# Optimization experiments

Hardware: AMD Instinct MI355X
Metric: run time of the kernel (lower is better)

Reference implementation:

```python
import jax, jax.numpy as jnp
import numpy as np

RADIUS = 0.2  # radius_cutoff
EPS_H = 1e-6
EPS_T = 1e-8
NUM_KNOTS = 16


def setup_inputs() -> dict:
    key = jax.random.key(0)
    ks = jax.random.split(key, 10)
    B, N, C = 2, 48 * 48, 16
    x = jax.random.normal(ks[0], (B, N, C), jnp.float32)
    phi_w1 = jax.random.normal(ks[1], (4, 32), jnp.float32) * 0.5
    phi_b1 = jax.random.normal(ks[2], (32,), jnp.float32) * 0.1
    phi_w2 = jax.random.normal(ks[3], (32, 1), jnp.float32) * 0.2
    phi_b2 = jax.random.normal(ks[4], (1,), jnp.float32) * 0.1
    h_w1 = jax.random.normal(ks[5], (2, 32), jnp.float32) * 0.5
    h_b1 = jax.random.normal(ks[6], (32,), jnp.float32) * 0.1
    h_w2 = jax.random.normal(ks[7], (32, 1), jnp.float32) * 0.2
    h_b2 = jax.random.normal(ks[8], (1,), jnp.float32) * 0.1
    S_m = jax.random.normal(ks[9], (NUM_KNOTS,), jnp.float32)
    return dict(x=x, phi_w1=phi_w1, phi_b1=phi_b1, phi_w2=phi_w2, phi_b2=phi_b2,
                h_w1=h_w1, h_b1=h_b1, h_w2=h_w2, h_b2=h_b2, S_m=S_m)


def _radial_spline(r, S_m):
    K = S_m.shape[0]
    knots = jnp.linspace(0.0, 1.0, K)
    r = jnp.clip(r, 0.0, 1.0)
    idx = jnp.clip(jnp.floor(r * (K - 1)).astype(jnp.int32), 0, K - 2)
    t_k = knots[idx]
    t_k1 = knots[idx + 1]
    wr = (r - t_k) / (t_k1 - t_k + EPS_T)
    return (1.0 - wr) * S_m[idx] + wr * S_m[idx + 1]


def reference(x, phi_w1, phi_b1, phi_w2, phi_b2, h_w1, h_b1, h_w2, h_b2, S_m):
    B, N, C = x.shape
    H = int(N ** 0.5)
    lin = jnp.linspace(0.0, 1.0, H)
    gx, gy = jnp.meshgrid(lin, lin, indexing='ij')
    coords = jnp.stack([gx, gy], axis=-1).reshape(N, 2)  # identical for every batch element

    # dense pairwise distances + radius mask  [N, N]
    diff = coords[:, None, :] - coords[None, :, :]
    dist = jnp.sqrt(jnp.sum(diff * diff, axis=-1))
    mask = (dist <= RADIUS).astype(x.dtype)

    # h_net: per-query bandwidth, Softplus(Linear(ReLU(Linear(coords))))  [N]
    h = jax.nn.softplus(jax.nn.relu(coords @ h_w1 + h_b1) @ h_w2 + h_b2)[:, 0]
    r_scaled = dist / (h[:, None] + EPS_H)
    psi = _radial_spline(r_scaled, S_m) * mask  # [N, N]

    # phi_net on all (x_i, y_j) coord pairs; original only fills masked entries,
    # elsewhere phi stays 0 -> dense eval then mask is the same math.  [N, N]
    xy = jnp.concatenate([jnp.broadcast_to(coords[:, None, :], (N, N, 2)),
                          jnp.broadcast_to(coords[None, :, :], (N, N, 2))], axis=-1)
    phi = (jax.nn.relu(xy @ phi_w1 + phi_b1) @ phi_w2 + phi_b2)[..., 0] * mask

    weights = phi * psi  # [N, N], same for every batch element
    norm = jnp.maximum(jnp.sum(mask, axis=-1, keepdims=True), 1.0)  # [N, 1]
    # sum_j weights[i,j] * x[b,j,c] / norm[i]  -- avoids materializing [B,N,N,C]
    out = jnp.einsum('ij,bjc->bic', weights, x) / norm[None, :, :]
    return out
```

## Files before the change

kernel.cpp:

```cpp
#include <hip/hip_runtime.h>
#include <cmath>

namespace {
constexpr int HG = 48;
constexpr int NP = HG * HG;
constexpr int CH = 16;
constexpr int WIN = 19;
constexpr int WIN2 = WIN * WIN;
constexpr float RADIUS = 0.2f;
constexpr float EPS_H = 1e-6f;
constexpr float EPS_T = 1e-8f;
constexpr int KNOTS = 16;
}

__device__ __forceinline__ float lin48(int t) {
    return (t == HG - 1) ? 1.0f : (float)t * (1.0f / (float)(HG - 1));
}

__device__ __forceinline__ float softplus_f(float v) {
    return fmaxf(v, 0.0f) + log1pf(expf(-fabsf(v)));
}

__global__ __launch_bounds__(256)
void si_blocks_kernel(const float* __restrict__ x,
                      const float* __restrict__ phi_w1,
                      const float* __restrict__ phi_b1,
                      const float* __restrict__ phi_w2,
                      const float* __restrict__ phi_b2,
                      const float* __restrict__ h_w1,
                      const float* __restrict__ h_b1,
                      const float* __restrict__ h_w2,
                      const float* __restrict__ h_b2,
                      const float* __restrict__ S_m,
                      float* __restrict__ out)
{
    const int i = blockIdx.x;
    const int tid = threadIdx.x;
    const int ri = i / HG;
    const int ci = i - ri * HG;
    const float xi = lin48(ri);
    const float yi = lin48(ci);

    __shared__ float4 s_q[32];
    __shared__ float  s_Sm[KNOTS];
    __shared__ float  s_h;
    __shared__ float  s_b2;

    if (tid < 32) {
        const float w0 = phi_w1[tid];
        const float w1 = phi_w1[32 + tid];
        const float pre = xi * w0 + yi * w1 + phi_b1[tid];
        s_q[tid] = make_float4(pre, phi_w1[64 + tid], phi_w1[96 + tid], phi_w2[tid]);
    } else if (tid < 48) {
        s_Sm[tid - 32] = S_m[tid - 32];
    } else if (tid == 64) {
        float hv = h_b2[0];
        #pragma unroll
        for (int k = 0; k < 32; ++k) {
            float t = xi * h_w1[k] + yi * h_w1[32 + k] + h_b1[k];
            t = fmaxf(t, 0.0f);
            hv = fmaf(t, h_w2[k], hv);
        }
        s_h = softplus_f(hv) + EPS_H;
        s_b2 = phi_b2[0];
    }
    __syncthreads();

    const float hval = s_h;
    const float b2 = s_b2;

    float acc[2][CH];
    #pragma unroll
    for (int b = 0; b < 2; ++b)
        #pragma unroll
        for (int c = 0; c < CH; ++c) acc[b][c] = 0.0f;
    float cnt = 0.0f;

    for (int t = tid; t < WIN2; t += 256) {
        const int a = t / WIN;
        const int bb = t - a * WIN;
        const int rj = ri + a - 9;
        const int cj = ci + bb - 9;
        if ((unsigned)rj >= (unsigned)HG || (unsigned)cj >= (unsigned)HG) continue;
        const float xj = lin48(rj);
        const float yj = lin48(cj);
        const float dx = xi - xj;
        const float dy = yi - yj;
        const float dist = sqrtf(dx * dx + dy * dy);
        if (dist > RADIUS) continue;
        cnt += 1.0f;

        float p = b2;
        #pragma unroll
        for (int k = 0; k < 32; ++k) {
            const float4 q = s_q[k];
            float hk = fmaf(xj, q.y, fmaf(yj, q.z, q.x));
            hk = fmaxf(hk, 0.0f);
            p = fmaf(hk, q.w, p);
        }

        float r = dist / hval;
        r = fminf(fmaxf(r, 0.0f), 1.0f);
        int idx = (int)(r * (float)(KNOTS - 1));
        idx = idx > (KNOTS - 2) ? (KNOTS - 2) : idx;
        const float tk  = (float)idx * (1.0f / (float)(KNOTS - 1));
        const float tk1 = (idx == KNOTS - 2) ? 1.0f
                        : (float)(idx + 1) * (1.0f / (float)(KNOTS - 1));
        const float wr = (r - tk) / (tk1 - tk + EPS_T);
        const float psi = (1.0f - wr) * s_Sm[idx] + wr * s_Sm[idx + 1];

        const float w = p * psi;
        const int j = rj * HG + cj;
        const float* xp0 = x + (size_t)j * CH;
        const float* xp1 = xp0 + (size_t)NP * CH;
        #pragma unroll
        for (int c = 0; c < CH; ++c) acc[0][c] = fmaf(w, xp0[c], acc[0][c]);
        #pragma unroll
        for (int c = 0; c < CH; ++c) acc[1][c] = fmaf(w, xp1[c], acc[1][c]);
    }

    #pragma unroll
    for (int off = 32; off > 0; off >>= 1) {
        #pragma unroll
        for (int b = 0; b < 2; ++b)
            #pragma unroll
            for (int c = 0; c < CH; ++c)
                acc[b][c] += __shfl_down(acc[b][c], off, 64);
        cnt += __shfl_down(cnt, off, 64);
    }

    __shared__ float s_red[4][33];
    const int lane = tid & 63;
    const int wv = tid >> 6;
    if (lane == 0) {
        #pragma unroll
        for (int b = 0; b < 2; ++b)
            #pragma unroll
            for (int c = 0; c < CH; ++c)
                s_red[wv][b * CH + c] = acc[b][c];
        s_red[wv][32] = cnt;
    }
    __syncthreads();

    if (tid < 32) {
        const float tot = s_red[0][tid] + s_red[1][tid] + s_red[2][tid] + s_red[3][tid];
        const float cn  = s_red[0][32] + s_red[1][32] + s_red[2][32] + s_red[3][32];
        const float norm = fmaxf(cn, 1.0f);
        const int b = tid >> 4;
        const int c = tid & 15;
        out[(size_t)b * NP * CH + (size_t)i * CH + c] = tot / norm;
    }
}

extern "C" void kernel_launch(void* const* d_in, const int* in_sizes, int n_in,
                              void* d_out, int out_size, void* d_ws, size_t ws_size,
                              hipStream_t stream) {
    const float* x      = (const float*)d_in[0];
    const float* phi_w1 = (const float*)d_in[1];
    const float* phi_b1 = (const float*)d_in[2];
    const float* phi_w2 = (const float*)d_in[3];
    const float* phi_b2 = (const float*)d_in[4];
    const float* h_w1   = (const float*)d_in[5];
    const float* h_b1   = (const float*)d_in[6];
    const float* h_w2   = (const float*)d_in[7];
    const float* h_b2   = (const float*)d_in[8];
    const float* S_m    = (const float*)d_in[9];
    float* out          = (float*)d_out;

    si_blocks_kernel<<<dim3(NP), dim3(256), 0, stream>>>(
        x, phi_w1, phi_b1, phi_w2, phi_b2,
        h_w1, h_b1, h_w2, h_b2, S_m, out);
}
```

Before: 100.1 us.

## Map one wavefront per query point and split weight compute from gather

Each 256-thread block now handles four query points, one wavefront each. Every lane computes weights for up to six window candidates without branching, storing the weight and byte offset in shared memory. A second phase has lanes gather float4 slices of x across batch and channel, and reduces the partial sums with a short shuffle tree. This targets idle threads in the 361-entry window, the divergent continue branches, the scalar per-channel loads and the heavy 32-channel shuffle reduction. The cost is more shared memory and registers per thread, plus work spent on masked-out candidates.

```diff
diff --git a/kernel.cpp b/kernel.cpp
--- a/kernel.cpp
+++ b/kernel.cpp
@@ -11,6 +11,8 @@
 constexpr float EPS_H = 1e-6f;
 constexpr float EPS_T = 1e-8f;
 constexpr int KNOTS = 16;
+constexpr int PPB = 4;
+constexpr int NCAND = 6;
 }
 
 __device__ __forceinline__ float lin48(int t) {
@@ -34,121 +36,139 @@
                       const float* __restrict__ S_m,
                       float* __restrict__ out)
 {
-    const int i = blockIdx.x;
-    const int tid = threadIdx.x;
-    const int ri = i / HG;
-    const int ci = i - ri * HG;
+    const int tid  = threadIdx.x;
+    const int lane = tid & 63;
+    const int p    = tid >> 6;
+    const int i    = blockIdx.x * PPB + p;
+    const int ri   = i / HG;
+    const int ci   = i - ri * HG;
     const float xi = lin48(ri);
     const float yi = lin48(ci);
 
-    __shared__ float4 s_q[32];
+    __shared__ float4 s_pq[PPB][32];
+    __shared__ float2 s_wj[PPB][WIN2];
     __shared__ float  s_Sm[KNOTS];
-    __shared__ float  s_h;
-    __shared__ float  s_b2;
 
-    if (tid < 32) {
-        const float w0 = phi_w1[tid];
-        const float w1 = phi_w1[32 + tid];
-        const float pre = xi * w0 + yi * w1 + phi_b1[tid];
-        s_q[tid] = make_float4(pre, phi_w1[64 + tid], phi_w1[96 + tid], phi_w2[tid]);
-    } else if (tid < 48) {
-        s_Sm[tid - 32] = S_m[tid - 32];
-    } else if (tid == 64) {
-        float hv = h_b2[0];
+    if (tid < 128) {
+        const int pb = tid >> 5;
+        const int k  = tid & 31;
+        const int ib = blockIdx.x * PPB + pb;
+        const int rb = ib / HG;
+        const int cb = ib - rb * HG;
+        const float xb = lin48(rb);
+        const float yb = lin48(cb);
+        const float pre = xb * phi_w1[k] + yb * phi_w1[32 + k] + phi_b1[k];
+        s_pq[pb][k] = make_float4(pre, phi_w1[64 + k], phi_w1[96 + k], phi_w2[k]);
+    } else if (tid < 128 + KNOTS) {
+        s_Sm[tid - 128] = S_m[tid - 128];
+    }
+
+    float hval;
+    {
+        const int k = lane & 31;
+        float tk = fmaxf(xi * h_w1[k] + yi * h_w1[32 + k] + h_b1[k], 0.0f) * h_w2[k];
         #pragma unroll
-        for (int k = 0; k < 32; ++k) {
-            float t = xi * h_w1[k] + yi * h_w1[32 + k] + h_b1[k];
-            t = fmaxf(t, 0.0f);
-            hv = fmaf(t, h_w2[k], hv);
-        }
-        s_h = softplus_f(hv) + EPS_H;
-        s_b2 = phi_b2[0];
+        for (int m = 1; m < 32; m <<= 1) tk += __shfl_xor(tk, m, 64);
+        hval = softplus_f(tk + h_b2[0]) + EPS_H;
     }
+    const float b2 = phi_b2[0];
+
     __syncthreads();
 
-    const float hval = s_h;
-    const float b2 = s_b2;
-
-    float acc[2][CH];
-    #pragma unroll
-    for (int b = 0; b < 2; ++b)
-        #pragma unroll
-        for (int c = 0; c < CH; ++c) acc[b][c] = 0.0f;
+    float xj[NCAND], yj[NCAND], pw[NCAND], accp[NCAND];
+    int joff[NCAND];
     float cnt = 0.0f;
 
-    for (int t = tid; t < WIN2; t += 256) {
-        const int a = t / WIN;
-        const int bb = t - a * WIN;
+    #pragma unroll
+    for (int s = 0; s < NCAND; ++s) {
+        const int t  = lane + 64 * s;
+        const bool in = (t < WIN2);
+        const int tt = in ? t : 0;
+        const int a  = tt / WIN;
+        const int bb = tt - a * WIN;
         const int rj = ri + a - 9;
         const int cj = ci + bb - 9;
-        if ((unsigned)rj >= (unsigned)HG || (unsigned)cj >= (unsigned)HG) continue;
-        const float xj = lin48(rj);
-        const float yj = lin48(cj);
-        const float dx = xi - xj;
-        const float dy = yi - yj;
+        const bool valid = in && ((unsigned)rj < (unsigned)HG) && ((unsigned)cj < (unsigned)HG);
+        const int rjc = min(max(rj, 0), HG - 1);
+        const int cjc = min(max(cj, 0), HG - 1);
+        const float xjv = lin48(rjc);
+        const float yjv = lin48(cjc);
+        const float dx = xi - xjv;
+        const float dy = yi - yjv;
         const float dist = sqrtf(dx * dx + dy * dy);
-        if (dist > RADIUS) continue;
-        cnt += 1.0f;
+        const float m = (valid && dist <= RADIUS) ? 1.0f : 0.0f;
+        cnt += m;
 
-        float p = b2;
-        #pragma unroll
-        for (int k = 0; k < 32; ++k) {
-            const float4 q = s_q[k];
-            float hk = fmaf(xj, q.y, fmaf(yj, q.z, q.x));
-            hk = fmaxf(hk, 0.0f);
-            p = fmaf(hk, q.w, p);
-        }
-
-        float r = dist / hval;
-        r = fminf(fmaxf(r, 0.0f), 1.0f);
+        float r = fminf(dist / hval, 1.0f);
         int idx = (int)(r * (float)(KNOTS - 1));
         idx = idx > (KNOTS - 2) ? (KNOTS - 2) : idx;
         const float tk  = (float)idx * (1.0f / (float)(KNOTS - 1));
         const float tk1 = (idx == KNOTS - 2) ? 1.0f
                         : (float)(idx + 1) * (1.0f / (float)(KNOTS - 1));
-        const float wr = (r - tk) / (tk1 - tk + EPS_T);
+        const float wr  = (r - tk) / (tk1 - tk + EPS_T);
         const float psi = (1.0f - wr) * s_Sm[idx] + wr * s_Sm[idx + 1];
 
-        const float w = p * psi;
-        const int j = rj * HG + cj;
-        const float* xp0 = x + (size_t)j * CH;
-        const float* xp1 = xp0 + (size_t)NP * CH;
-        #pragma unroll
-        for (int c = 0; c < CH; ++c) acc[0][c] = fmaf(w, xp0[c], acc[0][c]);
-        #pragma unroll
-        for (int c = 0; c < CH; ++c) acc[1][c] = fmaf(w, xp1[c], acc[1][c]);
+        pw[s]   = psi * m;
+        xj[s]   = xjv;
+        yj[s]   = yjv;
+        accp[s] = b2;
+        joff[s] = (rjc * HG + cjc) * 64;
     }
 
     #pragma unroll
-    for (int off = 32; off > 0; off >>= 1) {
+    for (int m = 1; m < 64; m <<= 1) cnt += __shfl_xor(cnt, m, 64);
+    const float rnorm = 1.0f / fmaxf(cnt, 1.0f);
+
+    #pragma unroll
+    for (int k = 0; k < 32; ++k) {
+        const float4 q = s_pq[p][k];
         #pragma unroll
-        for (int b = 0; b < 2; ++b)
-            #pragma unroll
-            for (int c = 0; c < CH; ++c)
-                acc[b][c] += __shfl_down(acc[b][c], off, 64);
-        cnt += __shfl_down(cnt, off, 64);
+        for (int s = 0; s < NCAND; ++s) {
+            float hk = fmaf(xj[s], q.y, fmaf(yj[s], q.z, q.x));
+            hk = fmaxf(hk, 0.0f);
+            accp[s] = fmaf(hk, q.w, accp[s]);
+        }
     }
 
-    __shared__ float s_red[4][33];
-    const int lane = tid & 63;
-    const int wv = tid >> 6;
-    if (lane == 0) {
-        #pragma unroll
-        for (int b = 0; b < 2; ++b)
-            #pragma unroll
-            for (int c = 0; c < CH; ++c)
-                s_red[wv][b * CH + c] = acc[b][c];
-        s_red[wv][32] = cnt;
+    #pragma unroll
+    for (int s = 0; s < NCAND; ++s) {
+        const int t = lane + 64 * s;
+        if (t < WIN2) {
+            const float w = accp[s] * pw[s] * rnorm;
+            s_wj[p][t] = make_float2(w, __int_as_float(joff[s]));
+        }
     }
+
     __syncthreads();
 
-    if (tid < 32) {
-        const float tot = s_red[0][tid] + s_red[1][tid] + s_red[2][tid] + s_red[3][tid];
-        const float cn  = s_red[0][32] + s_red[1][32] + s_red[2][32] + s_red[3][32];
-        const float norm = fmaxf(cn, 1.0f);
-        const int b = tid >> 4;
-        const int c = tid & 15;
-        out[(size_t)b * NP * CH + (size_t)i * CH + c] = tot / norm;
+    const int rep = (lane >> 3) & 7;
+    const int pc  = lane & 7;
+    const int b   = pc >> 2;
+    const int c4  = pc & 3;
+    const char* xbase = (const char*)x + (size_t)(b * NP * CH + c4 * 4) * 4;
+
+    float4 acc = make_float4(0.0f, 0.0f, 0.0f, 0.0f);
+    #pragma unroll 4
+    for (int t = rep; t < WIN2; t += 8) {
+        const float2 wj = s_wj[p][t];
+        const float4 xv = *(const float4*)(xbase + __float_as_int(wj.y));
+        acc.x = fmaf(wj.x, xv.x, acc.x);
+        acc.y = fmaf(wj.x, xv.y, acc.y);
+        acc.z = fmaf(wj.x, xv.z, acc.z);
+        acc.w = fmaf(wj.x, xv.w, acc.w);
+    }
+
+    #pragma unroll
+    for (int off = 8; off < 64; off <<= 1) {
+        acc.x += __shfl_down(acc.x, off, 64);
+        acc.y += __shfl_down(acc.y, off, 64);
+        acc.z += __shfl_down(acc.z, off, 64);
+        acc.w += __shfl_down(acc.w, off, 64);
+    }
+
+    if (rep == 0) {
+        float4* op = (float4*)(out + (size_t)(b * NP + i) * CH + c4 * 4);
+        *op = acc;
     }
 }
 
@@ -167,7 +187,7 @@
     const float* S_m    = (const float*)d_in[9];
     float* out          = (float*)d_out;
 
-    si_blocks_kernel<<<dim3(NP), dim3(256), 0, stream>>>(
+    si_blocks_kernel<<<dim3(NP / PPB), dim3(256), 0, stream>>>(
         x, phi_w1, phi_b1, phi_w2, phi_b2,
         h_w1, h_b1, h_w2, h_b2, S_m, out);
 }
```

New measurement: 84.82 us. 15.3% less time.
